# Kernel tuning notes

Measured on AMD Instinct MI355X. Metric: run time of the kernel, lower is better.

## Reference

```python
import jax, jax.numpy as jnp
import numpy as np
from jax import lax

B, T, C = 8, 2048, 1024
H, N = 16, 64          # n_head, head_size (C = H*N)
FFN = 3584             # dim_ffn = int(1024*3.5//32*32)
HSD = 8.0              # head_size_divisor
EPS = 1e-5


def setup_inputs() -> dict:
    key = jax.random.key(0)
    ks = jax.random.split(key, 24)
    s = 0.02
    return {
        'x': jax.random.normal(ks[0], (B, T, C), jnp.float32),
        'ln0_w': jnp.ones((C,), jnp.float32), 'ln0_b': jnp.zeros((C,), jnp.float32),
        'ln1_w': jnp.ones((C,), jnp.float32), 'ln1_b': jnp.zeros((C,), jnp.float32),
        'ln2_w': jnp.ones((C,), jnp.float32), 'ln2_b': jnp.zeros((C,), jnp.float32),
        'att_tmk': jax.random.uniform(ks[1], (C,), jnp.float32),
        'att_tmv': jax.random.uniform(ks[2], (C,), jnp.float32),
        'att_tmr': jax.random.uniform(ks[3], (C,), jnp.float32),
        'att_tmg': jax.random.uniform(ks[4], (C,), jnp.float32),
        'att_decay': jax.random.uniform(ks[5], (H, N), jnp.float32, -6.0, -1.0),
        'att_faaaa': jax.random.normal(ks[6], (H, N), jnp.float32) * 0.1,
        'att_Wr': jax.random.normal(ks[7], (C, C), jnp.float32) * s,
        'att_Wk': jax.random.normal(ks[8], (C, C), jnp.float32) * s,
        'att_Wv': jax.random.normal(ks[9], (C, C), jnp.float32) * s,
        'att_Wg': jax.random.normal(ks[10], (C, C), jnp.float32) * s,
        'att_Wo': jax.random.normal(ks[11], (C, C), jnp.float32) * s,
        'att_lnx_w': jnp.ones((C,), jnp.float32), 'att_lnx_b': jnp.zeros((C,), jnp.float32),
        'ffn_tmk': jax.random.uniform(ks[12], (C,), jnp.float32),
        'ffn_tmr': jax.random.uniform(ks[13], (C,), jnp.float32),
        'ffn_Wk': jax.random.normal(ks[14], (FFN, C), jnp.float32) * s,
        'ffn_Wr': jax.random.normal(ks[15], (C, C), jnp.float32) * s,
        'ffn_Wv': jax.random.normal(ks[16], (C, FFN), jnp.float32) * s,
    }


def token_shift(x):
    # nn.ZeroPad2d((0,0,1,-1)): shift right by one along T with zero front pad
    return jnp.pad(x, ((0, 0), (1, 0), (0, 0)))[:, :-1, :]


def layer_norm(x, w, b):
    mu = jnp.mean(x, -1, keepdims=True)
    var = jnp.var(x, -1, keepdims=True)
    return (x - mu) * lax.rsqrt(var + EPS) * w + b


def group_norm(x, w, b):
    # GroupNorm(H groups) over channel dim C = H*N
    xg = x.reshape(*x.shape[:-1], H, N)
    mu = jnp.mean(xg, -1, keepdims=True)
    var = jnp.var(xg, -1, keepdims=True)
    xg = (xg - mu) * lax.rsqrt(var + EPS)
    return xg.reshape(x.shape) * w + b


def wkv5(r, k, v, w, u):
    # r,k,v: [B,T,C]; w,u: [H,N]. Per-head decayed linear attention recurrence.
    ew = jnp.exp(-jnp.exp(w))  # [H,N] decay in (0,1)
    rt = r.reshape(B, T, H, N).transpose(1, 0, 2, 3)  # [T,B,H,N]
    kt = k.reshape(B, T, H, N).transpose(1, 0, 2, 3)
    vt = v.reshape(B, T, H, N).transpose(1, 0, 2, 3)

    def step(S, rkv):
        r_, k_, v_ = rkv                                   # [B,H,N]
        a = k_[..., :, None] * v_[..., None, :]            # [B,H,N,N] outer k v^T
        y = jnp.einsum('bhi,bhij->bhj', r_, S + u[:, :, None] * a)
        S = ew[None, :, :, None] * S + a
        return S, y

    S0 = jnp.zeros((B, H, N, N), r.dtype)
    _, ys = lax.scan(step, S0, (rt, kt, vt))               # ys: [T,B,H,N]
    return ys.transpose(1, 0, 2, 3).reshape(B, T, C)


def reference(x, ln0_w, ln0_b, ln1_w, ln1_b, ln2_w, ln2_b,
              att_tmk, att_tmv, att_tmr, att_tmg, att_decay, att_faaaa,
              att_Wr, att_Wk, att_Wv, att_Wg, att_Wo, att_lnx_w, att_lnx_b,
              ffn_tmk, ffn_tmr, ffn_Wk, ffn_Wr, ffn_Wv):
    x = layer_norm(x, ln0_w, ln0_b)  # layer_id == 0

    # --- time-mix (RWKV_Tmix_x052) ---
    xn = layer_norm(x, ln1_w, ln1_b)
    xx = token_shift(xn)
    xk = xn * att_tmk + xx * (1 - att_tmk)
    xv = xn * att_tmv + xx * (1 - att_tmv)
    xr = xn * att_tmr + xx * (1 - att_tmr)
    xg = xn * att_tmg + xx * (1 - att_tmg)
    r = xr @ att_Wr.T
    k = xk @ att_Wk.T
    v = xv @ att_Wv.T
    g = jax.nn.silu(xg @ att_Wg.T)
    y = wkv5(r, k, v, att_decay, att_faaaa)
    y = group_norm(y / HSD, att_lnx_w, att_lnx_b)
    x = x + (y * g) @ att_Wo.T

    # --- channel-mix (RWKV_CMix_x052) ---
    xn = layer_norm(x, ln2_w, ln2_b)
    xx = token_shift(xn)
    xk = xn * ffn_tmk + xx * (1 - ffn_tmk)
    xr = xn * ffn_tmr + xx * (1 - ffn_tmr)
    kf = jnp.square(jax.nn.relu(xk @ ffn_Wk.T))
    kv = kf @ ffn_Wv.T
    x = x + jax.nn.sigmoid(xr @ ffn_Wr.T) * kv
    return x
```

## Files before the change

kernel.cpp:

```cpp
#include <hip/hip_runtime.h>

#define Bq 8
#define Tq 2048
#define Cq 1024
#define Hq 16
#define Nq 64
#define FFNq 3584
#define EPSq 1e-5f

typedef __bf16 bf8v __attribute__((ext_vector_type(8)));
typedef float f32x4 __attribute__((ext_vector_type(4)));

typedef __attribute__((address_space(1))) const unsigned int GU;
typedef __attribute__((address_space(3))) unsigned int LU;

__device__ __forceinline__ void gload16(const unsigned short* g, unsigned short* l) {
    __builtin_amdgcn_global_load_lds((GU*)g, (LU*)l, 16, 0, 0);
}

__device__ __forceinline__ unsigned short f2bf(float f) {
    unsigned u = __float_as_uint(f);
    u += 0x7fffu + ((u >> 16) & 1u);
    return (unsigned short)(u >> 16);
}
__device__ __forceinline__ float bf2f(unsigned short h) {
    return __uint_as_float(((unsigned)h) << 16);
}

__global__ __launch_bounds__(256)
void diag_kernel(float* __restrict__ out, float val) {
    int i = (blockIdx.x * 256 + threadIdx.x) * 4;
    float4 v = make_float4(val, val, val, val);
    *(float4*)(out + i) = v;
}

__global__ __launch_bounds__(256)
void f2bf_all_kernel(const float* __restrict__ s0, const float* __restrict__ s1,
                     const float* __restrict__ s2, const float* __restrict__ s3,
                     const float* __restrict__ s4, const float* __restrict__ s5,
                     const float* __restrict__ s6, const float* __restrict__ s7,
                     unsigned short* __restrict__ d0, unsigned short* __restrict__ d1,
                     unsigned short* __restrict__ d2, unsigned short* __restrict__ d3,
                     unsigned short* __restrict__ d4, unsigned short* __restrict__ d5,
                     unsigned short* __restrict__ d6, unsigned short* __restrict__ d7) {
    int b = blockIdx.x;
    const float* src; unsigned short* dst;
    if      (b < 1024)  { src = s0; dst = d0; }
    else if (b < 2048)  { src = s1; dst = d1; b -= 1024; }
    else if (b < 3072)  { src = s2; dst = d2; b -= 2048; }
    else if (b < 4096)  { src = s3; dst = d3; b -= 3072; }
    else if (b < 5120)  { src = s4; dst = d4; b -= 4096; }
    else if (b < 8704)  { src = s5; dst = d5; b -= 5120; }
    else if (b < 9728)  { src = s6; dst = d6; b -= 8704; }
    else                { src = s7; dst = d7; b -= 9728; }
    int i = (b * 256 + threadIdx.x) * 4;
    float4 v = *(const float4*)(src + i);
    ushort4 o;
    o.x = f2bf(v.x); o.y = f2bf(v.y); o.z = f2bf(v.z); o.w = f2bf(v.w);
    *(ushort4*)(dst + i) = o;
}

__device__ __forceinline__ void blockred2(float& a, float& b, float* sm) {
#pragma unroll
    for (int m = 1; m < 64; m <<= 1) { a += __shfl_xor(a, m); b += __shfl_xor(b, m); }
    const int w = threadIdx.x >> 6;
    __syncthreads();
    if ((threadIdx.x & 63) == 0) { sm[w] = a; sm[4 + w] = b; }
    __syncthreads();
    a = sm[0] + sm[1] + sm[2] + sm[3];
    b = sm[4] + sm[5] + sm[6] + sm[7];
}

__global__ __launch_bounds__(256)
void ln01_kernel(const float* __restrict__ x,
                 const float* __restrict__ w0, const float* __restrict__ b0,
                 const float* __restrict__ w1, const float* __restrict__ b1,
                 float* __restrict__ x0, unsigned short* __restrict__ xn) {
    __shared__ float sm[8];
    const int tok = blockIdx.x, tid = threadIdx.x, c = tid * 4;
    const size_t base = (size_t)tok * Cq + c;
    float4 v = *(const float4*)(x + base);
    float s = v.x + v.y + v.z + v.w;
    float ss = v.x * v.x + v.y * v.y + v.z * v.z + v.w * v.w;
    blockred2(s, ss, sm);
    float mu = s * (1.f / Cq);
    float rstd = rsqrtf(ss * (1.f / Cq) - mu * mu + EPSq);
    float4 wv = *(const float4*)(w0 + c), bv = *(const float4*)(b0 + c);
    float4 e;
    e.x = (v.x - mu) * rstd * wv.x + bv.x;
    e.y = (v.y - mu) * rstd * wv.y + bv.y;
    e.z = (v.z - mu) * rstd * wv.z + bv.z;
    e.w = (v.w - mu) * rstd * wv.w + bv.w;
    *(float4*)(x0 + base) = e;
    s = e.x + e.y + e.z + e.w;
    ss = e.x * e.x + e.y * e.y + e.z * e.z + e.w * e.w;
    blockred2(s, ss, sm);
    mu = s * (1.f / Cq);
    rstd = rsqrtf(ss * (1.f / Cq) - mu * mu + EPSq);
    wv = *(const float4*)(w1 + c); bv = *(const float4*)(b1 + c);
    ushort4 o;
    o.x = f2bf((e.x - mu) * rstd * wv.x + bv.x);
    o.y = f2bf((e.y - mu) * rstd * wv.y + bv.y);
    o.z = f2bf((e.z - mu) * rstd * wv.z + bv.z);
    o.w = f2bf((e.w - mu) * rstd * wv.w + bv.w);
    *(ushort4*)(xn + base) = o;
}

__global__ __launch_bounds__(256)
void ln_kernel(const float* __restrict__ x, const float* __restrict__ w,
               const float* __restrict__ b, unsigned short* __restrict__ out) {
    __shared__ float sm[8];
    const int tok = blockIdx.x, tid = threadIdx.x, c = tid * 4;
    const size_t base = (size_t)tok * Cq + c;
    float4 v = *(const float4*)(x + base);
    float s = v.x + v.y + v.z + v.w;
    float ss = v.x * v.x + v.y * v.y + v.z * v.z + v.w * v.w;
    blockred2(s, ss, sm);
    float mu = s * (1.f / Cq);
    float rstd = rsqrtf(ss * (1.f / Cq) - mu * mu + EPSq);
    float4 wv = *(const float4*)(w + c), bv = *(const float4*)(b + c);
    ushort4 o;
    o.x = f2bf((v.x - mu) * rstd * wv.x + bv.x);
    o.y = f2bf((v.y - mu) * rstd * wv.y + bv.y);
    o.z = f2bf((v.z - mu) * rstd * wv.z + bv.z);
    o.w = f2bf((v.w - mu) * rstd * wv.w + bv.w);
    *(ushort4*)(out + base) = o;
}

__device__ __forceinline__ ushort4 mixpack(float ax, float ay, float az, float aw,
                                           float px, float py, float pz, float pw,
                                           const float4& m) {
    ushort4 o;
    o.x = f2bf(px + m.x * (ax - px));
    o.y = f2bf(py + m.y * (ay - py));
    o.z = f2bf(pz + m.z * (az - pz));
    o.w = f2bf(pw + m.w * (aw - pw));
    return o;
}

__global__ __launch_bounds__(256)
void mix4_kernel(const unsigned short* __restrict__ xn,
                 const float* __restrict__ tmr, const float* __restrict__ tmk,
                 const float* __restrict__ tmv, const float* __restrict__ tmg,
                 ushort4* __restrict__ outR, ushort4* __restrict__ outK,
                 ushort4* __restrict__ outV, ushort4* __restrict__ outG) {
    const int tok = blockIdx.x, tid = threadIdx.x, c = tid * 4;
    const int t = tok & (Tq - 1);
    const size_t base = (size_t)tok * Cq + c;
    ushort4 a = *(const ushort4*)(xn + base);
    ushort4 p = make_ushort4(0, 0, 0, 0);
    if (t) p = *(const ushort4*)(xn + base - Cq);
    float ax = bf2f(a.x), ay = bf2f(a.y), az = bf2f(a.z), aw = bf2f(a.w);
    float px = bf2f(p.x), py = bf2f(p.y), pz = bf2f(p.z), pw = bf2f(p.w);
    const size_t b4 = (size_t)tok * 256 + tid;
    outR[b4] = mixpack(ax, ay, az, aw, px, py, pz, pw, *(const float4*)(tmr + c));
    outK[b4] = mixpack(ax, ay, az, aw, px, py, pz, pw, *(const float4*)(tmk + c));
    outV[b4] = mixpack(ax, ay, az, aw, px, py, pz, pw, *(const float4*)(tmv + c));
    outG[b4] = mixpack(ax, ay, az, aw, px, py, pz, pw, *(const float4*)(tmg + c));
}

__global__ __launch_bounds__(256)
void mix2_kernel(const unsigned short* __restrict__ xn,
                 const float* __restrict__ tmk, const float* __restrict__ tmr,
                 ushort4* __restrict__ outK, ushort4* __restrict__ outR) {
    const int tok = blockIdx.x, tid = threadIdx.x, c = tid * 4;
    const int t = tok & (Tq - 1);
    const size_t base = (size_t)tok * Cq + c;
    ushort4 a = *(const ushort4*)(xn + base);
    ushort4 p = make_ushort4(0, 0, 0, 0);
    if (t) p = *(const ushort4*)(xn + base - Cq);
    float ax = bf2f(a.x), ay = bf2f(a.y), az = bf2f(a.z), aw = bf2f(a.w);
    float px = bf2f(p.x), py = bf2f(p.y), pz = bf2f(p.z), pw = bf2f(p.w);
    const size_t b4 = (size_t)tok * 256 + tid;
    outK[b4] = mixpack(ax, ay, az, aw, px, py, pz, pw, *(const float4*)(tmk + c));
    outR[b4] = mixpack(ax, ay, az, aw, px, py, pz, pw, *(const float4*)(tmr + c));
}

template<int MODE>
__global__ __launch_bounds__(512, 2)
void gemm256(const unsigned short* __restrict__ A, const unsigned short* __restrict__ W,
             int K, int N, float* __restrict__ outF, unsigned short* __restrict__ outB,
             const float* __restrict__ res, const unsigned short* __restrict__ sg) {
    __shared__ unsigned short lds[8][8192];
    const int tid = threadIdx.x;
    const int wid = tid >> 6, lane = tid & 63;
    const int wr = wid >> 2, wc = wid & 3;
    const int l15 = lane & 15, q = lane >> 4;

    const int nn = N >> 8;
    const int q8 = gridDim.x >> 3;
    const int bid = blockIdx.x;
    const int swz = (bid & 7) * q8 + (bid >> 3);
    const int m0 = (swz / nn) * 256;
    const int n0 = (swz % nn) * 256;

    const int srow = tid >> 2;
    const int scol = ((tid & 3) ^ ((tid >> 2) & 3)) * 8;
    const unsigned short* aS0 = A + (size_t)(m0 + srow) * K + scol;
    const unsigned short* aS1 = A + (size_t)(m0 + 128 + srow) * K + scol;
    const unsigned short* wS0 = W + (size_t)(n0 + srow) * K + scol;
    const unsigned short* wS1 = W + (size_t)(n0 + 128 + srow) * K + scol;

    const int fco = (q ^ (l15 & 3)) * 8;
    const int aOff = (wr * 128 + l15) * 32 + fco;
    const int bOff = (wc * 64 + l15) * 32 + fco;

    f32x4 acc[8][4];
#pragma unroll
    for (int mi = 0; mi < 8; ++mi)
#pragma unroll
        for (int ni = 0; ni < 4; ++ni)
            acc[mi][ni] = {0.f, 0.f, 0.f, 0.f};

    const int NJ = K >> 5;

#pragma unroll
    for (int j = 0; j < 3; ++j) {
        unsigned short* La = &lds[j][tid * 8];
        unsigned short* Lb = &lds[4 + j][tid * 8];
        gload16(aS0 + j * 32, La); gload16(aS1 + j * 32, La + 4096);
        gload16(wS0 + j * 32, Lb); gload16(wS1 + j * 32, Lb + 4096);
    }
    asm volatile("s_waitcnt vmcnt(8)" ::: "memory");
    __builtin_amdgcn_s_barrier();

    bf8v a[4], b[4];
    for (int k = 0; k < NJ; ++k) {
        const int rg = k & 3;
        const unsigned short* LA = &lds[rg][0];
        const unsigned short* LB = &lds[4 + rg][0];
        const bool st = (k + 3) < NJ;
        const int sj = (k + 3) & 3;

        if (st) {
            unsigned short* La = &lds[sj][tid * 8];
            gload16(aS0 + (k + 3) * 32, La);
            gload16(aS1 + (k + 3) * 32, La + 4096);
        }
#pragma unroll
        for (int i = 0; i < 4; ++i) a[i] = *(const bf8v*)&LA[aOff + i * 512];
#pragma unroll
        for (int i = 0; i < 4; ++i) b[i] = *(const bf8v*)&LB[bOff + i * 512];
        __builtin_amdgcn_s_barrier();
        asm volatile("s_waitcnt lgkmcnt(0)" ::: "memory");
        __builtin_amdgcn_sched_barrier(0);
        __builtin_amdgcn_s_setprio(1);
#pragma unroll
        for (int mi = 0; mi < 4; ++mi)
#pragma unroll
            for (int ni = 0; ni < 4; ++ni)
                acc[mi][ni] = __builtin_amdgcn_mfma_f32_16x16x32_bf16(a[mi], b[ni], acc[mi][ni], 0, 0, 0);
        __builtin_amdgcn_s_setprio(0);
        __builtin_amdgcn_s_barrier();

        if (st) {
            unsigned short* Lb = &lds[4 + sj][tid * 8];
            gload16(wS0 + (k + 3) * 32, Lb);
            gload16(wS1 + (k + 3) * 32, Lb + 4096);
        }
#pragma unroll
        for (int i = 0; i < 4; ++i) a[i] = *(const bf8v*)&LA[aOff + (4 + i) * 512];
        __builtin_amdgcn_s_barrier();
        asm volatile("s_waitcnt lgkmcnt(0)" ::: "memory");
        __builtin_amdgcn_sched_barrier(0);
        __builtin_amdgcn_s_setprio(1);
#pragma unroll
        for (int mi = 0; mi < 4; ++mi)
#pragma unroll
            for (int ni = 0; ni < 4; ++ni)
                acc[4 + mi][ni] = __builtin_amdgcn_mfma_f32_16x16x32_bf16(a[mi], b[ni], acc[4 + mi][ni], 0, 0, 0);
        __builtin_amdgcn_s_setprio(0);
        if (k <= NJ - 4)      { asm volatile("s_waitcnt vmcnt(8)" ::: "memory"); }
        else if (k == NJ - 3) { asm volatile("s_waitcnt vmcnt(4)" ::: "memory"); }
        else if (k == NJ - 2) { asm volatile("s_waitcnt vmcnt(0)" ::: "memory"); }
        __builtin_amdgcn_s_barrier();
    }

#pragma unroll
    for (int mi = 0; mi < 8; ++mi)
#pragma unroll
        for (int ni = 0; ni < 4; ++ni)
#pragma unroll
            for (int j = 0; j < 4; ++j) {
                const int row = m0 + wr * 128 + mi * 16 + q * 4 + j;
                const int col = n0 + wc * 64 + ni * 16 + l15;
                const size_t idx = (size_t)row * N + col;
                const float av = acc[mi][ni][j];
                if (MODE == 1) {
                    outB[idx] = f2bf(av / (1.f + __expf(-av)));
                } else if (MODE == 2) {
                    outF[idx] = res[idx] + av;
                } else if (MODE == 3) {
                    float tt = fmaxf(av, 0.f);
                    outB[idx] = f2bf(tt * tt);
                } else if (MODE == 4) {
                    outB[idx] = f2bf(1.f / (1.f + __expf(-av)));
                } else if (MODE == 5) {
                    outF[idx] = res[idx] + bf2f(sg[idx]) * av;
                } else {
                    outB[idx] = f2bf(av);
                }
            }
}

__global__ __launch_bounds__(256)
void wkv_kernel(const unsigned short* __restrict__ r, const unsigned short* __restrict__ k,
                const unsigned short* __restrict__ v, const unsigned short* __restrict__ g,
                const float* __restrict__ decay, const float* __restrict__ faaaa,
                const float* __restrict__ lnxw, const float* __restrict__ lnxb,
                unsigned short* __restrict__ ao) {
    __shared__ unsigned short rp[64 * 72], km[64 * 72], kdT[64 * 72];
    __shared__ unsigned short VT[64 * 72], Abf[64 * 72], ScT[64 * 72], Gsh[64 * 72];
    __shared__ float Dt[64];
    const int tid = threadIdx.x;
    const int bh = blockIdx.x, b = bh >> 4, h = bh & 15;
    const int tr = tid >> 2, g4 = tid & 3, i0 = g4 * 16;
    const int wv = tid >> 6, lane = tid & 63, l15 = lane & 15, q = lane >> 4;
    const float LOG2E = 1.44269504088896340736f;

    float l2w[16], uu[16];
#pragma unroll
    for (int ii = 0; ii < 16; ++ii) {
        l2w[ii] = -__expf(decay[h * Nq + i0 + ii]) * LOG2E;
        uu[ii] = faaaa[h * Nq + i0 + ii];
    }
    float ewL[4];
#pragma unroll
    for (int jr = 0; jr < 4; ++jr) {
        float lw = -__expf(decay[h * Nq + 16 * wv + q * 4 + jr]) * LOG2E;
        ewL[jr] = exp2f(64.f * lw);
    }
    const int colbase = h * Nq;
    float lwj[4], lbj[4];
#pragma unroll
    for (int nt = 0; nt < 4; ++nt) {
        lwj[nt] = lnxw[colbase + 16 * nt + l15];
        lbj[nt] = lnxb[colbase + 16 * nt + l15];
    }
    f32x4 S[4];
#pragma unroll
    for (int nt = 0; nt < 4; ++nt) S[nt] = {0.f, 0.f, 0.f, 0.f};
    for (int idx = tid; idx < 64 * 72; idx += 256) ScT[idx] = 0;
    __syncthreads();

    const size_t rowbase = (size_t)b * Tq;

    for (int c = 0; c < 32; ++c) {
        const size_t grow = (rowbase + c * 64 + tr) * Cq + colbase + i0;
        unsigned short rs_[16], ks_[16], vs_[16];
        *(uint4*)&rs_[0] = *(const uint4*)(r + grow);
        *(uint4*)&rs_[8] = *(const uint4*)(r + grow + 8);
        *(uint4*)&ks_[0] = *(const uint4*)(k + grow);
        *(uint4*)&ks_[8] = *(const uint4*)(k + grow + 8);
        *(uint4*)&vs_[0] = *(const uint4*)(v + grow);
        *(uint4*)&vs_[8] = *(const uint4*)(v + grow + 8);
        *(uint4*)&Gsh[tr * 72 + i0] = *(const uint4*)(g + grow);
        *(uint4*)&Gsh[tr * 72 + i0 + 8] = *(const uint4*)(g + grow + 8);
        float pd = 0.f;
        const float ftr = (float)tr;
#pragma unroll
        for (int ii = 0; ii < 16; ++ii) {
            float rf = bf2f(rs_[ii]), kf = bf2f(ks_[ii]);
            rp[tr * 72 + i0 + ii] = f2bf(rf * exp2f(ftr * l2w[ii]));
            km[tr * 72 + i0 + ii] = f2bf(kf * exp2f(-(ftr + 1.f) * l2w[ii]));
            kdT[(i0 + ii) * 72 + tr] = f2bf(kf * exp2f((63.f - ftr) * l2w[ii]));
            VT[(i0 + ii) * 72 + tr] = vs_[ii];
            pd += rf * uu[ii] * kf;
        }
        pd += __shfl_xor(pd, 1);
        pd += __shfl_xor(pd, 2);
        if (g4 == 0) Dt[tr] = pd;
        __syncthreads();

        f32x4 accA[4];
#pragma unroll
        for (int nt = 0; nt < 4; ++nt) accA[nt] = {0.f, 0.f, 0.f, 0.f};
#pragma unroll
        for (int ks = 0; ks < 2; ++ks) {
            bf8v a = *(const bf8v*)&rp[(16 * wv + l15) * 72 + ks * 32 + q * 8];
#pragma unroll
            for (int nt = 0; nt < 4; ++nt) {
                bf8v bbv = *(const bf8v*)&km[(16 * nt + l15) * 72 + ks * 32 + q * 8];
                accA[nt] = __builtin_amdgcn_mfma_f32_16x16x32_bf16(a, bbv, accA[nt], 0, 0, 0);
            }
        }
#pragma unroll
        for (int nt = 0; nt < 4; ++nt)
#pragma unroll
            for (int jr = 0; jr < 4; ++jr) {
                const int t = 16 * wv + q * 4 + jr, s = 16 * nt + l15;
                const float a = accA[nt][jr];
                const float val = (s < t) ? a : ((s == t) ? Dt[t] : 0.f);
                Abf[t * 72 + s] = f2bf(val);
            }

        f32x4 accY[4];
#pragma unroll
        for (int nt = 0; nt < 4; ++nt) accY[nt] = {0.f, 0.f, 0.f, 0.f};
#pragma unroll
        for (int ks = 0; ks < 2; ++ks) {
            bf8v a = *(const bf8v*)&Abf[(16 * wv + l15) * 72 + ks * 32 + q * 8];
#pragma unroll
            for (int nt = 0; nt < 4; ++nt) {
                bf8v bbv = *(const bf8v*)&VT[(16 * nt + l15) * 72 + ks * 32 + q * 8];
                accY[nt] = __builtin_amdgcn_mfma_f32_16x16x32_bf16(a, bbv, accY[nt], 0, 0, 0);
            }
        }
#pragma unroll
        for (int ks = 0; ks < 2; ++ks) {
            bf8v a = *(const bf8v*)&rp[(16 * wv + l15) * 72 + ks * 32 + q * 8];
#pragma unroll
            for (int nt = 0; nt < 4; ++nt) {
                bf8v bbv = *(const bf8v*)&ScT[(16 * nt + l15) * 72 + ks * 32 + q * 8];
                accY[nt] = __builtin_amdgcn_mfma_f32_16x16x32_bf16(a, bbv, accY[nt], 0, 0, 0);
            }
        }

        float sum_[4] = {0.f, 0.f, 0.f, 0.f}, sq_[4] = {0.f, 0.f, 0.f, 0.f};
#pragma unroll
        for (int nt = 0; nt < 4; ++nt)
#pragma unroll
            for (int jr = 0; jr < 4; ++jr) {
                float yv = accY[nt][jr] * 0.125f;
                accY[nt][jr] = yv;
                sum_[jr] += yv;
                sq_[jr] += yv * yv;
            }
#pragma unroll
        for (int m = 1; m < 16; m <<= 1)
#pragma unroll
            for (int jr = 0; jr < 4; ++jr) {
                sum_[jr] += __shfl_xor(sum_[jr], m);
                sq_[jr] += __shfl_xor(sq_[jr], m);
            }
        float mu_[4], rstd_[4];
#pragma unroll
        for (int jr = 0; jr < 4; ++jr) {
            mu_[jr] = sum_[jr] * (1.f / Nq);
            rstd_[jr] = rsqrtf(sq_[jr] * (1.f / Nq) - mu_[jr] * mu_[jr] + EPSq);
        }
#pragma unroll
        for (int nt = 0; nt < 4; ++nt)
#pragma unroll
            for (int jr = 0; jr < 4; ++jr) {
                const int t = 16 * wv + q * 4 + jr;
                const float gate = bf2f(Gsh[t * 72 + 16 * nt + l15]);
                const float val = (accY[nt][jr] - mu_[jr]) * rstd_[jr] * lwj[nt] + lbj[nt];
                ao[(rowbase + c * 64 + t) * Cq + colbase + 16 * nt + l15] = f2bf(val * gate);
            }

        f32x4 accU[4];
#pragma unroll
        for (int nt = 0; nt < 4; ++nt) accU[nt] = {0.f, 0.f, 0.f, 0.f};
#pragma unroll
        for (int ks = 0; ks < 2; ++ks) {
            bf8v a = *(const bf8v*)&kdT[(16 * wv + l15) * 72 + ks * 32 + q * 8];
#pragma unroll
            for (int nt = 0; nt < 4; ++nt) {
                bf8v bbv = *(const bf8v*)&VT[(16 * nt + l15) * 72 + ks * 32 + q * 8];
                accU[nt] = __builtin_amdgcn_mfma_f32_16x16x32_bf16(a, bbv, accU[nt], 0, 0, 0);
            }
        }
        __syncthreads();
#pragma unroll
        for (int nt = 0; nt < 4; ++nt) {
#pragma unroll
            for (int jr = 0; jr < 4; ++jr)
                S[nt][jr] = ewL[jr] * S[nt][jr] + accU[nt][jr];
            ushort4 sc;
            sc.x = f2bf(S[nt][0]); sc.y = f2bf(S[nt][1]);
            sc.z = f2bf(S[nt][2]); sc.w = f2bf(S[nt][3]);
            *(ushort4*)&ScT[(16 * nt + l15) * 72 + 16 * wv + q * 4] = sc;
        }
        __syncthreads();
    }
}

extern "C" void kernel_launch(void* const* d_in, const int* in_sizes, int n_in,
                              void* d_out, int out_size, void* d_ws, size_t ws_size,
                              hipStream_t stream) {
    const float* x     = (const float*)d_in[0];
    const float* ln0w  = (const float*)d_in[1];
    const float* ln0b  = (const float*)d_in[2];
    const float* ln1w  = (const float*)d_in[3];
    const float* ln1b  = (const float*)d_in[4];
    const float* ln2w  = (const float*)d_in[5];
    const float* ln2b  = (const float*)d_in[6];
    const float* atmk  = (const float*)d_in[7];
    const float* atmv  = (const float*)d_in[8];
    const float* atmr  = (const float*)d_in[9];
    const float* atmg  = (const float*)d_in[10];
    const float* decay = (const float*)d_in[11];
    const float* faaaa = (const float*)d_in[12];
    const float* aWr   = (const float*)d_in[13];
    const float* aWk   = (const float*)d_in[14];
    const float* aWv   = (const float*)d_in[15];
    const float* aWg   = (const float*)d_in[16];
    const float* aWo   = (const float*)d_in[17];
    const float* lnxw  = (const float*)d_in[18];
    const float* lnxb  = (const float*)d_in[19];
    const float* ftmk  = (const float*)d_in[20];
    const float* ftmr  = (const float*)d_in[21];
    const float* fWk   = (const float*)d_in[22];
    const float* fWr   = (const float*)d_in[23];
    const float* fWv   = (const float*)d_in[24];

    const size_t MB = 1024ull * 1024ull;
    const size_t WS_NEEDED = 250 * MB;
    dim3 blk(256);

    if (ws_size < WS_NEEDED) {
        diag_kernel<<<out_size / 1024, blk, 0, stream>>>((float*)d_out,
            1000.f + (float)((double)ws_size / (double)MB));
        return;
    }

    char* ws = (char*)d_ws;
    unsigned short* WR  = (unsigned short*)(ws + 0 * MB);
    unsigned short* WK  = (unsigned short*)(ws + 2 * MB);
    unsigned short* WV  = (unsigned short*)(ws + 4 * MB);
    unsigned short* WG  = (unsigned short*)(ws + 6 * MB);
    unsigned short* WO  = (unsigned short*)(ws + 8 * MB);
    unsigned short* FWK = (unsigned short*)(ws + 10 * MB);
    unsigned short* FWR = (unsigned short*)(ws + 17 * MB);
    unsigned short* FWV = (unsigned short*)(ws + 19 * MB);
    unsigned short* XN  = (unsigned short*)(ws + 26 * MB);
    unsigned short* MXR = (unsigned short*)(ws + 58 * MB);
    unsigned short* MXK = (unsigned short*)(ws + 90 * MB);
    unsigned short* MXV = (unsigned short*)(ws + 122 * MB);
    unsigned short* MXG = (unsigned short*)(ws + 154 * MB);
    unsigned short* Rb  = (unsigned short*)(ws + 186 * MB);
    unsigned short* Kb  = (unsigned short*)(ws + 58 * MB);
    unsigned short* Vb  = (unsigned short*)(ws + 90 * MB);
    unsigned short* Gb  = (unsigned short*)(ws + 122 * MB);
    unsigned short* AO  = (unsigned short*)(ws + 154 * MB);
    unsigned short* XK2 = (unsigned short*)(ws + 58 * MB);
    unsigned short* XR2 = (unsigned short*)(ws + 90 * MB);
    unsigned short* KF  = (unsigned short*)(ws + 122 * MB);
    unsigned short* SRb = (unsigned short*)(ws + 26 * MB);
    float*          X0  = (float*)d_out;

    const int NTOK = Bq * Tq;
    dim3 blk512(512);
    const int gsq = (NTOK / 256) * (Cq / 256);
    const int gup = (NTOK / 256) * (FFNq / 256);

    f2bf_all_kernel<<<13312, blk, 0, stream>>>(aWr, aWk, aWv, aWg, aWo, fWk, fWr, fWv,
                                               WR, WK, WV, WG, WO, FWK, FWR, FWV);

    ln01_kernel<<<NTOK, blk, 0, stream>>>(x, ln0w, ln0b, ln1w, ln1b, X0, XN);

    mix4_kernel<<<NTOK, blk, 0, stream>>>(XN, atmr, atmk, atmv, atmg,
                                          (ushort4*)MXR, (ushort4*)MXK,
                                          (ushort4*)MXV, (ushort4*)MXG);

    gemm256<6><<<gsq, blk512, 0, stream>>>(MXR, WR, Cq, Cq, nullptr, Rb, nullptr, nullptr);
    gemm256<6><<<gsq, blk512, 0, stream>>>(MXK, WK, Cq, Cq, nullptr, Kb, nullptr, nullptr);
    gemm256<6><<<gsq, blk512, 0, stream>>>(MXV, WV, Cq, Cq, nullptr, Vb, nullptr, nullptr);
    gemm256<1><<<gsq, blk512, 0, stream>>>(MXG, WG, Cq, Cq, nullptr, Gb, nullptr, nullptr);

    wkv_kernel<<<Bq * Hq, blk, 0, stream>>>(Rb, Kb, Vb, Gb, decay, faaaa, lnxw, lnxb, AO);
    gemm256<2><<<gsq, blk512, 0, stream>>>(AO, WO, Cq, Cq, X0, nullptr, X0, nullptr);

    ln_kernel<<<NTOK, blk, 0, stream>>>(X0, ln2w, ln2b, XN);
    mix2_kernel<<<NTOK, blk, 0, stream>>>(XN, ftmk, ftmr, (ushort4*)XK2, (ushort4*)XR2);
    gemm256<3><<<gup, blk512, 0, stream>>>(XK2, FWK, Cq, FFNq, nullptr, KF, nullptr, nullptr);
    gemm256<4><<<gsq, blk512, 0, stream>>>(XR2, FWR, Cq, Cq, nullptr, SRb, nullptr, nullptr);
    gemm256<5><<<gsq, blk512, 0, stream>>>(KF, FWV, FFNq, Cq, X0, nullptr, X0, SRb);
}
```

Baseline: 963.4 us.

## Shrink GEMM tile to 256x128 with triple-buffered LDS and one barrier per step

```diff
diff --git a/kernel.cpp b/kernel.cpp
--- a/kernel.cpp
+++ b/kernel.cpp
@@ -177,37 +177,36 @@
 }
 
 template<int MODE>
-__global__ __launch_bounds__(512, 2)
-void gemm256(const unsigned short* __restrict__ A, const unsigned short* __restrict__ W,
+__global__ __launch_bounds__(512, 4)
+void gemm128(const unsigned short* __restrict__ A, const unsigned short* __restrict__ W,
              int K, int N, float* __restrict__ outF, unsigned short* __restrict__ outB,
              const float* __restrict__ res, const unsigned short* __restrict__ sg) {
-    __shared__ unsigned short lds[8][8192];
+    __shared__ unsigned short lds[3][12288];
     const int tid = threadIdx.x;
     const int wid = tid >> 6, lane = tid & 63;
-    const int wr = wid >> 2, wc = wid & 3;
+    const int wr = wid >> 1, wc = wid & 1;
     const int l15 = lane & 15, q = lane >> 4;
 
-    const int nn = N >> 8;
+    const int nn = N >> 7;
     const int q8 = gridDim.x >> 3;
     const int bid = blockIdx.x;
     const int swz = (bid & 7) * q8 + (bid >> 3);
     const int m0 = (swz / nn) * 256;
-    const int n0 = (swz % nn) * 256;
+    const int n0 = (swz % nn) * 128;
 
     const int srow = tid >> 2;
     const int scol = ((tid & 3) ^ ((tid >> 2) & 3)) * 8;
     const unsigned short* aS0 = A + (size_t)(m0 + srow) * K + scol;
     const unsigned short* aS1 = A + (size_t)(m0 + 128 + srow) * K + scol;
-    const unsigned short* wS0 = W + (size_t)(n0 + srow) * K + scol;
-    const unsigned short* wS1 = W + (size_t)(n0 + 128 + srow) * K + scol;
+    const unsigned short* wS  = W + (size_t)(n0 + srow) * K + scol;
 
     const int fco = (q ^ (l15 & 3)) * 8;
-    const int aOff = (wr * 128 + l15) * 32 + fco;
-    const int bOff = (wc * 64 + l15) * 32 + fco;
-
-    f32x4 acc[8][4];
-#pragma unroll
-    for (int mi = 0; mi < 8; ++mi)
+    const int aOff = (wr * 64 + l15) * 32 + fco;
+    const int bOff = 8192 + (wc * 64 + l15) * 32 + fco;
+
+    f32x4 acc[4][4];
+#pragma unroll
+    for (int mi = 0; mi < 4; ++mi)
 #pragma unroll
         for (int ni = 0; ni < 4; ++ni)
             acc[mi][ni] = {0.f, 0.f, 0.f, 0.f};
@@ -215,35 +214,29 @@
     const int NJ = K >> 5;
 
 #pragma unroll
-    for (int j = 0; j < 3; ++j) {
-        unsigned short* La = &lds[j][tid * 8];
-        unsigned short* Lb = &lds[4 + j][tid * 8];
-        gload16(aS0 + j * 32, La); gload16(aS1 + j * 32, La + 4096);
-        gload16(wS0 + j * 32, Lb); gload16(wS1 + j * 32, Lb + 4096);
-    }
-    asm volatile("s_waitcnt vmcnt(8)" ::: "memory");
+    for (int j = 0; j < 2; ++j) {
+        gload16(aS0 + j * 32, &lds[j][tid * 8]);
+        gload16(aS1 + j * 32, &lds[j][4096 + tid * 8]);
+        gload16(wS  + j * 32, &lds[j][8192 + tid * 8]);
+    }
+    asm volatile("s_waitcnt vmcnt(3)" ::: "memory");
     __builtin_amdgcn_s_barrier();
 
-    bf8v a[4], b[4];
+    unsigned short* L0 = &lds[0][0];
+    unsigned short* L1 = &lds[1][0];
+    unsigned short* L2 = &lds[2][0];
+
     for (int k = 0; k < NJ; ++k) {
-        const int rg = k & 3;
-        const unsigned short* LA = &lds[rg][0];
-        const unsigned short* LB = &lds[4 + rg][0];
-        const bool st = (k + 3) < NJ;
-        const int sj = (k + 3) & 3;
-
-        if (st) {
-            unsigned short* La = &lds[sj][tid * 8];
-            gload16(aS0 + (k + 3) * 32, La);
-            gload16(aS1 + (k + 3) * 32, La + 4096);
-        }
-#pragma unroll
-        for (int i = 0; i < 4; ++i) a[i] = *(const bf8v*)&LA[aOff + i * 512];
-#pragma unroll
-        for (int i = 0; i < 4; ++i) b[i] = *(const bf8v*)&LB[bOff + i * 512];
-        __builtin_amdgcn_s_barrier();
-        asm volatile("s_waitcnt lgkmcnt(0)" ::: "memory");
-        __builtin_amdgcn_sched_barrier(0);
+        if (k + 2 < NJ) {
+            gload16(aS0 + (k + 2) * 32, L2 + tid * 8);
+            gload16(aS1 + (k + 2) * 32, L2 + 4096 + tid * 8);
+            gload16(wS  + (k + 2) * 32, L2 + 8192 + tid * 8);
+        }
+        bf8v a[4], b[4];
+#pragma unroll
+        for (int i = 0; i < 4; ++i) a[i] = *(const bf8v*)&L0[aOff + i * 512];
+#pragma unroll
+        for (int i = 0; i < 4; ++i) b[i] = *(const bf8v*)&L0[bOff + i * 512];
         __builtin_amdgcn_s_setprio(1);
 #pragma unroll
         for (int mi = 0; mi < 4; ++mi)
@@ -251,38 +244,23 @@
             for (int ni = 0; ni < 4; ++ni)
                 acc[mi][ni] = __builtin_amdgcn_mfma_f32_16x16x32_bf16(a[mi], b[ni], acc[mi][ni], 0, 0, 0);
         __builtin_amdgcn_s_setprio(0);
-        __builtin_amdgcn_s_barrier();
-
-        if (st) {
-            unsigned short* Lb = &lds[4 + sj][tid * 8];
-            gload16(wS0 + (k + 3) * 32, Lb);
-            gload16(wS1 + (k + 3) * 32, Lb + 4096);
-        }
-#pragma unroll
-        for (int i = 0; i < 4; ++i) a[i] = *(const bf8v*)&LA[aOff + (4 + i) * 512];
-        __builtin_amdgcn_s_barrier();
-        asm volatile("s_waitcnt lgkmcnt(0)" ::: "memory");
-        __builtin_amdgcn_sched_barrier(0);
-        __builtin_amdgcn_s_setprio(1);
-#pragma unroll
-        for (int mi = 0; mi < 4; ++mi)
-#pragma unroll
-            for (int ni = 0; ni < 4; ++ni)
-                acc[4 + mi][ni] = __builtin_amdgcn_mfma_f32_16x16x32_bf16(a[mi], b[ni], acc[4 + mi][ni], 0, 0, 0);
-        __builtin_amdgcn_s_setprio(0);
-        if (k <= NJ - 4)      { asm volatile("s_waitcnt vmcnt(8)" ::: "memory"); }
-        else if (k == NJ - 3) { asm volatile("s_waitcnt vmcnt(4)" ::: "memory"); }
-        else if (k == NJ - 2) { asm volatile("s_waitcnt vmcnt(0)" ::: "memory"); }
-        __builtin_amdgcn_s_barrier();
-    }
-
-#pragma unroll
-    for (int mi = 0; mi < 8; ++mi)
+        if (k < NJ - 2) {
+            asm volatile("s_waitcnt vmcnt(3)" ::: "memory");
+            __builtin_amdgcn_s_barrier();
+        } else if (k == NJ - 2) {
+            asm volatile("s_waitcnt vmcnt(0)" ::: "memory");
+            __builtin_amdgcn_s_barrier();
+        }
+        unsigned short* t0 = L0; L0 = L1; L1 = L2; L2 = t0;
+    }
+
+#pragma unroll
+    for (int mi = 0; mi < 4; ++mi)
 #pragma unroll
         for (int ni = 0; ni < 4; ++ni)
 #pragma unroll
             for (int j = 0; j < 4; ++j) {
-                const int row = m0 + wr * 128 + mi * 16 + q * 4 + j;
+                const int row = m0 + wr * 64 + mi * 16 + q * 4 + j;
                 const int col = n0 + wc * 64 + ni * 16 + l15;
                 const size_t idx = (size_t)row * N + col;
                 const float av = acc[mi][ni][j];
@@ -542,8 +520,8 @@
 
     const int NTOK = Bq * Tq;
     dim3 blk512(512);
-    const int gsq = (NTOK / 256) * (Cq / 256);
-    const int gup = (NTOK / 256) * (FFNq / 256);
+    const int gsq = (NTOK / 256) * (Cq / 128);
+    const int gup = (NTOK / 256) * (FFNq / 128);
 
     f2bf_all_kernel<<<13312, blk, 0, stream>>>(aWr, aWk, aWv, aWg, aWo, fWk, fWr, fWv,
                                                WR, WK, WV, WG, WO, FWK, FWR, FWV);
@@ -554,17 +532,17 @@
                                           (ushort4*)MXR, (ushort4*)MXK,
                                           (ushort4*)MXV, (ushort4*)MXG);
 
-    gemm256<6><<<gsq, blk512, 0, stream>>>(MXR, WR, Cq, Cq, nullptr, Rb, nullptr, nullptr);
-    gemm256<6><<<gsq, blk512, 0, stream>>>(MXK, WK, Cq, Cq, nullptr, Kb, nullptr, nullptr);
-    gemm256<6><<<gsq, blk512, 0, stream>>>(MXV, WV, Cq, Cq, nullptr, Vb, nullptr, nullptr);
-    gemm256<1><<<gsq, blk512, 0, stream>>>(MXG, WG, Cq, Cq, nullptr, Gb, nullptr, nullptr);
+    gemm128<6><<<gsq, blk512, 0, stream>>>(MXR, WR, Cq, Cq, nullptr, Rb, nullptr, nullptr);
+    gemm128<6><<<gsq, blk512, 0, stream>>>(MXK, WK, Cq, Cq, nullptr, Kb, nullptr, nullptr);
+    gemm128<6><<<gsq, blk512, 0, stream>>>(MXV, WV, Cq, Cq, nullptr, Vb, nullptr, nullptr);
+    gemm128<1><<<gsq, blk512, 0, stream>>>(MXG, WG, Cq, Cq, nullptr, Gb, nullptr, nullptr);
 
     wkv_kernel<<<Bq * Hq, blk, 0, stream>>>(Rb, Kb, Vb, Gb, decay, faaaa, lnxw, lnxb, AO);
-    gemm256<2><<<gsq, blk512, 0, stream>>>(AO, WO, Cq, Cq, X0, nullptr, X0, nullptr);
+    gemm128<2><<<gsq, blk512, 0, stream>>>(AO, WO, Cq, Cq, X0, nullptr, X0, nullptr);
 
     ln_kernel<<<NTOK, blk, 0, stream>>>(X0, ln2w, ln2b, XN);
     mix2_kernel<<<NTOK, blk, 0, stream>>>(XN, ftmk, ftmr, (ushort4*)XK2, (ushort4*)XR2);
-    gemm256<3><<<gup, blk512, 0, stream>>>(XK2, FWK, Cq, FFNq, nullptr, KF, nullptr, nullptr);
-    gemm256<4><<<gsq, blk512, 0, stream>>>(XR2, FWR, Cq, Cq, nullptr, SRb, nullptr, nullptr);
-    gemm256<5><<<gsq, blk512, 0, stream>>>(KF, FWV, FFNq, Cq, X0, nullptr, X0, SRb);
-}
+    gemm128<3><<<gup, blk512, 0, stream>>>(XK2, FWK, Cq, FFNq, nullptr, KF, nullptr, nullptr);
+    gemm128<4><<<gsq, blk512, 0, stream>>>(XR2, FWR, Cq, Cq, nullptr, SRb, nullptr, nullptr);
+    gemm128<5><<<gsq, blk512, 0, stream>>>(KF, FWV, FFNq, Cq, X0, nullptr, X0, SRb);
+}
```

Result: faster. 943.7 us (-2.1%).
